# Optimization experiments

Measured on AMD Instinct MI355X. Metric: run time of the kernel, lower is better.

The kernel has to match this reference:

```python
import jax, jax.numpy as jnp
import numpy as np

UNITS = 512
SENSORY = 256
BATCH = 256
ODE_UNFOLDS = 6
EPSILON = 1e-8
ELAPSED_TIME = 1.0


def setup_inputs() -> dict:
    key = jax.random.key(0)
    ks = jax.random.split(key, 16)
    u = lambda k, shape, lo, hi: jax.random.uniform(k, shape, jnp.float32, lo, hi)
    pm1 = lambda k, shape: (jax.random.randint(k, shape, 0, 2).astype(jnp.float32) * 2.0 - 1.0)
    return {
        "x": jax.random.normal(ks[0], (BATCH, SENSORY), jnp.float32),
        "state": jax.random.normal(ks[1], (BATCH, UNITS), jnp.float32),
        "gleak": u(ks[2], (UNITS,), 0.001, 1.0),
        "vleak": u(ks[3], (UNITS,), -0.2, 0.2),
        "cm": u(ks[4], (UNITS,), 0.4, 0.6),
        "sigma": u(ks[5], (UNITS, UNITS), 3.0, 8.0),
        "mu": u(ks[6], (UNITS, UNITS), 0.3, 0.8),
        "w": u(ks[7], (UNITS, UNITS), 0.001, 1.0),
        "erev": pm1(ks[8], (UNITS, UNITS)),
        "sensory_sigma": u(ks[9], (SENSORY, UNITS), 3.0, 8.0),
        "sensory_mu": u(ks[10], (SENSORY, UNITS), 0.3, 0.8),
        "sensory_w": u(ks[11], (SENSORY, UNITS), 0.001, 1.0),
        "sensory_erev": pm1(ks[12], (SENSORY, UNITS)),
        "input_w": jnp.ones((SENSORY,), jnp.float32),
        "input_b": jnp.zeros((SENSORY,), jnp.float32),
        "output_w": jnp.ones((UNITS,), jnp.float32),
        "output_b": jnp.zeros((UNITS,), jnp.float32),
    }


def _gate(v_pre, mu, sigma):
    # v_pre: (B, P) broadcast against (P, Q) params -> (B, P, Q)
    return jax.nn.sigmoid(sigma * (v_pre[:, :, None] - mu))


def reference(x, state, gleak, vleak, cm, sigma, mu, w, erev,
              sensory_sigma, sensory_mu, sensory_w, sensory_erev,
              input_w, input_b, output_w, output_b):
    inputs = x * input_w + input_b  # (B, D)
    sens_act = sensory_w * _gate(inputs, sensory_mu, sensory_sigma)  # (B, D, N)
    w_num_sensory = jnp.sum(sens_act * sensory_erev, axis=1)  # (B, N)
    w_den_sensory = jnp.sum(sens_act, axis=1)                 # (B, N)

    cm_t = cm / ((ELAPSED_TIME + 0.001) / ODE_UNFOLDS)  # (N,)
    v_pre = state
    for _ in range(ODE_UNFOLDS):
        w_act = w * _gate(v_pre, mu, sigma)               # (B, N, N)
        w_num = jnp.sum(w_act * erev, axis=1) + w_num_sensory
        w_den = jnp.sum(w_act, axis=1) + w_den_sensory
        numerator = cm_t * v_pre + gleak * vleak + w_num
        denominator = cm_t + gleak + w_den
        v_pre = numerator / (denominator + EPSILON)

    outputs = v_pre * output_w + output_b
    return outputs, v_pre
```

## Files before the change

### kernel.cpp

```cpp
#include <hip/hip_runtime.h>

#define UNITS 512
#define SENSD 256
#define BATCH 256
#define BN (BATCH * UNITS)
#define LOG2E 1.44269504088896340736f
#define CMF (6.0f / 1.001f)

__device__ __forceinline__ float frcp(float x)  { return __builtin_amdgcn_rcpf(x); }
__device__ __forceinline__ float fexp2(float x) { return __builtin_amdgcn_exp2f(x); }

__global__ __launch_bounds__(256) void prep_kernel(
    const float* __restrict__ sigma, const float* __restrict__ mu,
    const float* __restrict__ w, const float* __restrict__ erev,
    const float* __restrict__ ssig, const float* __restrict__ smu,
    const float* __restrict__ sw, const float* __restrict__ serev,
    const float* __restrict__ gleak, const float* __restrict__ vleak,
    const float* __restrict__ cm,
    float4* __restrict__ fusedR, float4* __restrict__ fusedS,
    float4* __restrict__ cmg) {
  int idx = blockIdx.x * 256 + threadIdx.x;
  if (idx < UNITS * UNITS) {
    float s = sigma[idx], m = mu[idx], ww = w[idx], e = erev[idx];
    fusedR[idx] = make_float4(-s * LOG2E, s * m * LOG2E, ww, ww * e);
  } else {
    int j = idx - UNITS * UNITS;
    if (j < SENSD * UNITS) {
      float s = ssig[j], m = smu[j], ww = sw[j], e = serev[j];
      fusedS[j] = make_float4(-s * LOG2E, s * m * LOG2E, ww, ww * e);
    }
  }
  if (idx < UNITS) {
    float cmt = cm[idx] * CMF, gl = gleak[idx];
    cmg[idx] = make_float4(cmt, gl * vleak[idx], cmt + gl + 1e-8f, 0.f);
  }
}

__global__ __launch_bounds__(256) void sensory_kernel(
    const float* __restrict__ x, const float* __restrict__ in_w, const float* __restrict__ in_b,
    const float4* __restrict__ fusedS,
    float* __restrict__ snf, float* __restrict__ sdf) {
  __shared__ float xl[8][128];
  int bi = blockIdx.x;
  int phs = bi & 1, qt = (bi >> 1) & 7, bt = bi >> 4;
  int tid = threadIdx.x;
  for (int i = tid; i < 1024; i += 256) {
    int br = i >> 7, dl = i & 127;
    int d = phs * 128 + dl;
    xl[br][dl] = fmaf(x[(bt * 8 + br) * SENSD + d], in_w[d], in_b[d]);
  }
  __syncthreads();
  int ql = tid & 63, bg = tid >> 6;
  int q = qt * 64 + ql;
  int r0 = bg * 2;
  const float4* F = fusedS + (size_t)(phs * 128) * UNITS + q;
  float n0 = 0.f, dn0 = 0.f, n1 = 0.f, dn1 = 0.f;
  #pragma unroll 8
  for (int dd = 0; dd < 128; ++dd) {
    float4 f = F[(size_t)dd * UNITS];
    float v0 = xl[r0][dd], v1 = xl[r0 + 1][dd];
    float u0 = 1.0f + fexp2(fmaf(f.x, v0, f.y));
    float u1 = 1.0f + fexp2(fmaf(f.x, v1, f.y));
    float r = frcp(u0 * u1);
    float m = f.w * r, k = f.z * r;
    n0 = fmaf(m, u1, n0);  dn0 = fmaf(k, u1, dn0);
    n1 = fmaf(m, u0, n1);  dn1 = fmaf(k, u0, dn1);
  }
  int bp0 = (bt * 8 + r0) * UNITS + q;
  size_t o = (size_t)phs * BN + bp0;
  snf[o] = n0;         sdf[o] = dn0;
  snf[o + UNITS] = n1; sdf[o + UNITS] = dn1;
}

__global__ __launch_bounds__(256, 4) void unfold_kernel(
    const float4* __restrict__ fusedR, const float* __restrict__ vprev,
    const float* __restrict__ pn_in, const float* __restrict__ pd_in,
    const float* __restrict__ snf, const float* __restrict__ sdf,
    const float4* __restrict__ cmg,
    float* __restrict__ vout,
    float* __restrict__ pn_out, float* __restrict__ pd_out,
    int first) {
  __shared__ float vl[64][20];
  int bi = blockIdx.x;
  int ph = bi & 7, qt = (bi >> 3) & 7, bt = bi >> 6;
  int tid = threadIdx.x;
  if (first) {
    for (int i = tid; i < 1024; i += 256) {
      int br = i >> 6, pl = i & 63;
      vl[pl][br] = vprev[(bt * 16 + br) * UNITS + ph * 64 + pl];
    }
  } else {
    for (int i = tid; i < 1024; i += 256) {
      int br = i >> 6, pl = i & 63;
      int p = ph * 64 + pl;
      int bp = (bt * 16 + br) * UNITS + p;
      float num = ((pn_in[bp] + pn_in[BN + bp]) + (pn_in[2 * BN + bp] + pn_in[3 * BN + bp]))
                + ((pn_in[4 * BN + bp] + pn_in[5 * BN + bp]) + (pn_in[6 * BN + bp] + pn_in[7 * BN + bp]))
                + (snf[bp] + snf[BN + bp]);
      float den = ((pd_in[bp] + pd_in[BN + bp]) + (pd_in[2 * BN + bp] + pd_in[3 * BN + bp]))
                + ((pd_in[4 * BN + bp] + pd_in[5 * BN + bp]) + (pd_in[6 * BN + bp] + pd_in[7 * BN + bp]))
                + (sdf[bp] + sdf[BN + bp]);
      float4 c = cmg[p];
      float v = fmaf(c.x, vprev[bp], c.y + num) * frcp(c.z + den);
      vl[pl][br] = v;
      if (qt == 0) vout[bp] = v;
    }
  }
  __syncthreads();
  int ql = tid & 63, bg = tid >> 6;
  int q = qt * 64 + ql;
  int r0 = bg * 4;
  const float4* F = fusedR + (size_t)(ph * 64) * UNITS + q;
  float n0 = 0.f, n1 = 0.f, n2 = 0.f, n3 = 0.f;
  float d0 = 0.f, d1 = 0.f, d2 = 0.f, d3 = 0.f;
  #pragma unroll 8
  for (int pp = 0; pp < 64; ++pp) {
    float4 f = F[(size_t)pp * UNITS];
    float4 vv = *(const float4*)&vl[pp][r0];
    float u0 = 1.0f + fexp2(fmaf(f.x, vv.x, f.y));
    float u1 = 1.0f + fexp2(fmaf(f.x, vv.y, f.y));
    float u2 = 1.0f + fexp2(fmaf(f.x, vv.z, f.y));
    float u3 = 1.0f + fexp2(fmaf(f.x, vv.w, f.y));
    float rA = frcp(u0 * u1);
    float rB = frcp(u2 * u3);
    float mA = f.w * rA, kA = f.z * rA;
    float mB = f.w * rB, kB = f.z * rB;
    n0 = fmaf(mA, u1, n0);  d0 = fmaf(kA, u1, d0);
    n1 = fmaf(mA, u0, n1);  d1 = fmaf(kA, u0, d1);
    n2 = fmaf(mB, u3, n2);  d2 = fmaf(kB, u3, d2);
    n3 = fmaf(mB, u2, n3);  d3 = fmaf(kB, u2, d3);
  }
  int bp = (bt * 16 + r0) * UNITS + q;
  size_t o = (size_t)ph * BN + bp;
  pn_out[o] = n0;             pd_out[o] = d0;
  pn_out[o + UNITS] = n1;     pd_out[o + UNITS] = d1;
  pn_out[o + 2 * UNITS] = n2; pd_out[o + 2 * UNITS] = d2;
  pn_out[o + 3 * UNITS] = n3; pd_out[o + 3 * UNITS] = d3;
}

__global__ __launch_bounds__(256) void final_kernel(
    const float* __restrict__ vprev,
    const float* __restrict__ pn, const float* __restrict__ pd,
    const float* __restrict__ snf, const float* __restrict__ sdf,
    const float4* __restrict__ cmg,
    const float* __restrict__ ow, const float* __restrict__ ob,
    float* __restrict__ out) {
  int idx = blockIdx.x * 256 + threadIdx.x;
  if (idx >= BN) return;
  int p = idx & (UNITS - 1);
  float num = ((pn[idx] + pn[BN + idx]) + (pn[2 * BN + idx] + pn[3 * BN + idx]))
            + ((pn[4 * BN + idx] + pn[5 * BN + idx]) + (pn[6 * BN + idx] + pn[7 * BN + idx]))
            + (snf[idx] + snf[BN + idx]);
  float den = ((pd[idx] + pd[BN + idx]) + (pd[2 * BN + idx] + pd[3 * BN + idx]))
            + ((pd[4 * BN + idx] + pd[5 * BN + idx]) + (pd[6 * BN + idx] + pd[7 * BN + idx]))
            + (sdf[idx] + sdf[BN + idx]);
  float4 c = cmg[p];
  float v = fmaf(c.x, vprev[idx], c.y + num) * frcp(c.z + den);
  out[idx] = fmaf(v, ow[p], ob[p]);
  out[BN + idx] = v;
}

extern "C" void kernel_launch(void* const* d_in, const int* in_sizes, int n_in,
                              void* d_out, int out_size, void* d_ws, size_t ws_size,
                              hipStream_t stream) {
  (void)in_sizes; (void)n_in; (void)out_size; (void)ws_size;
  const float* x     = (const float*)d_in[0];
  const float* state = (const float*)d_in[1];
  const float* gleak = (const float*)d_in[2];
  const float* vleak = (const float*)d_in[3];
  const float* cm    = (const float*)d_in[4];
  const float* sigma = (const float*)d_in[5];
  const float* mu    = (const float*)d_in[6];
  const float* w     = (const float*)d_in[7];
  const float* erev  = (const float*)d_in[8];
  const float* ssig  = (const float*)d_in[9];
  const float* smu   = (const float*)d_in[10];
  const float* sw    = (const float*)d_in[11];
  const float* serev = (const float*)d_in[12];
  const float* in_w  = (const float*)d_in[13];
  const float* in_b  = (const float*)d_in[14];
  const float* out_w = (const float*)d_in[15];
  const float* out_b = (const float*)d_in[16];

  float* ws = (float*)d_ws;
  float4* fusedR = (float4*)(ws);
  float4* fusedS = (float4*)(ws + 1048576);
  float4* cmg    = (float4*)(ws + 1572864);
  float*  pnA    = ws + 1574912;
  float*  pdA    = ws + 2623488;
  float*  pnB    = ws + 3672064;
  float*  pdB    = ws + 4720640;
  float*  snf    = ws + 5769216;
  float*  sdf    = ws + 6031360;
  float*  vA     = ws + 6293504;
  float*  vB     = ws + 6424576;

  prep_kernel<<<1536, 256, 0, stream>>>(sigma, mu, w, erev, ssig, smu, sw, serev,
                                        gleak, vleak, cm, fusedR, fusedS, cmg);
  sensory_kernel<<<512, 256, 0, stream>>>(x, in_w, in_b, fusedS, snf, sdf);

  unfold_kernel<<<1024, 256, 0, stream>>>(fusedR, state, pnA, pdA, snf, sdf, cmg,
                                          vA, pnA, pdA, 1);
  unfold_kernel<<<1024, 256, 0, stream>>>(fusedR, state, pnA, pdA, snf, sdf, cmg,
                                          vA, pnB, pdB, 0);
  unfold_kernel<<<1024, 256, 0, stream>>>(fusedR, vA, pnB, pdB, snf, sdf, cmg,
                                          vB, pnA, pdA, 0);
  unfold_kernel<<<1024, 256, 0, stream>>>(fusedR, vB, pnA, pdA, snf, sdf, cmg,
                                          vA, pnB, pdB, 0);
  unfold_kernel<<<1024, 256, 0, stream>>>(fusedR, vA, pnB, pdB, snf, sdf, cmg,
                                          vB, pnA, pdA, 0);
  unfold_kernel<<<1024, 256, 0, stream>>>(fusedR, vB, pnA, pdA, snf, sdf, cmg,
                                          vA, pnB, pdB, 0);
  final_kernel<<<512, 256, 0, stream>>>(vA, pnB, pdB, snf, sdf, cmg,
                                        out_w, out_b, (float*)d_out);
}
```

Before: 161.2 us.

## Use packed FP32 FMAs with duplicated parameter layout in gate accumulation loops

Each gate parameter is now written twice (pairs duplicated into two float4 arrays), so the inner loops can use two-wide packed FMA (v_pk_fma_f32) over pairs of batch rows. The paired-reciprocal trick (one rcp for two gates plus extra multiplies) is replaced by one reciprocal per gate, relying on packed math to cut the VALU instruction count. In exchange, the parameter tensors double in size, so global/L2 traffic per iteration doubles, the unroll drops to 4, and twice as many transcendental rcp ops are issued.

```diff
diff --git a/kernel.cpp b/kernel.cpp
--- a/kernel.cpp
+++ b/kernel.cpp
@@ -7,8 +7,11 @@
 #define LOG2E 1.44269504088896340736f
 #define CMF (6.0f / 1.001f)
 
+typedef __attribute__((ext_vector_type(2))) float v2f;
+
 __device__ __forceinline__ float frcp(float x)  { return __builtin_amdgcn_rcpf(x); }
 __device__ __forceinline__ float fexp2(float x) { return __builtin_amdgcn_exp2f(x); }
+__device__ __forceinline__ v2f vfma(v2f a, v2f b, v2f c) { return __builtin_elementwise_fma(a, b, c); }
 
 __global__ __launch_bounds__(256) void prep_kernel(
     const float* __restrict__ sigma, const float* __restrict__ mu,
@@ -17,17 +20,22 @@
     const float* __restrict__ sw, const float* __restrict__ serev,
     const float* __restrict__ gleak, const float* __restrict__ vleak,
     const float* __restrict__ cm,
-    float4* __restrict__ fusedR, float4* __restrict__ fusedS,
+    float4* __restrict__ RA, float4* __restrict__ RB,
+    float4* __restrict__ SA, float4* __restrict__ SB,
     float4* __restrict__ cmg) {
   int idx = blockIdx.x * 256 + threadIdx.x;
   if (idx < UNITS * UNITS) {
     float s = sigma[idx], m = mu[idx], ww = w[idx], e = erev[idx];
-    fusedR[idx] = make_float4(-s * LOG2E, s * m * LOG2E, ww, ww * e);
+    float fx = -s * LOG2E, fy = s * m * LOG2E, we = ww * e;
+    RA[idx] = make_float4(fx, fx, fy, fy);
+    RB[idx] = make_float4(ww, ww, we, we);
   } else {
     int j = idx - UNITS * UNITS;
     if (j < SENSD * UNITS) {
       float s = ssig[j], m = smu[j], ww = sw[j], e = serev[j];
-      fusedS[j] = make_float4(-s * LOG2E, s * m * LOG2E, ww, ww * e);
+      float fx = -s * LOG2E, fy = s * m * LOG2E, we = ww * e;
+      SA[j] = make_float4(fx, fx, fy, fy);
+      SB[j] = make_float4(ww, ww, we, we);
     }
   }
   if (idx < UNITS) {
@@ -38,7 +46,7 @@
 
 __global__ __launch_bounds__(256) void sensory_kernel(
     const float* __restrict__ x, const float* __restrict__ in_w, const float* __restrict__ in_b,
-    const float4* __restrict__ fusedS,
+    const float4* __restrict__ SA, const float4* __restrict__ SB,
     float* __restrict__ snf, float* __restrict__ sdf) {
   __shared__ float xl[8][128];
   int bi = blockIdx.x;
@@ -53,27 +61,33 @@
   int ql = tid & 63, bg = tid >> 6;
   int q = qt * 64 + ql;
   int r0 = bg * 2;
-  const float4* F = fusedS + (size_t)(phs * 128) * UNITS + q;
-  float n0 = 0.f, dn0 = 0.f, n1 = 0.f, dn1 = 0.f;
-  #pragma unroll 8
+  const float4* FA = SA + (size_t)(phs * 128) * UNITS + q;
+  const float4* FB = SB + (size_t)(phs * 128) * UNITS + q;
+  const v2f one2 = {1.0f, 1.0f};
+  v2f n01 = {0.f, 0.f}, d01 = {0.f, 0.f};
+  #pragma unroll 4
   for (int dd = 0; dd < 128; ++dd) {
-    float4 f = F[(size_t)dd * UNITS];
-    float v0 = xl[r0][dd], v1 = xl[r0 + 1][dd];
-    float u0 = 1.0f + fexp2(fmaf(f.x, v0, f.y));
-    float u1 = 1.0f + fexp2(fmaf(f.x, v1, f.y));
-    float r = frcp(u0 * u1);
-    float m = f.w * r, k = f.z * r;
-    n0 = fmaf(m, u1, n0);  dn0 = fmaf(k, u1, dn0);
-    n1 = fmaf(m, u0, n1);  dn1 = fmaf(k, u0, dn1);
+    float4 fa = FA[(size_t)dd * UNITS];
+    float4 fb = FB[(size_t)dd * UNITS];
+    v2f fxx = {fa.x, fa.y}, fyy = {fa.z, fa.w};
+    v2f fzz = {fb.x, fb.y}, fww = {fb.z, fb.w};
+    v2f v01 = {xl[r0][dd], xl[r0 + 1][dd]};
+    v2f z01 = vfma(fxx, v01, fyy);
+    v2f t01; t01.x = fexp2(z01.x); t01.y = fexp2(z01.y);
+    v2f u01 = t01 + one2;
+    v2f s01; s01.x = frcp(u01.x); s01.y = frcp(u01.y);
+    n01 = vfma(fww, s01, n01);
+    d01 = vfma(fzz, s01, d01);
   }
   int bp0 = (bt * 8 + r0) * UNITS + q;
   size_t o = (size_t)phs * BN + bp0;
-  snf[o] = n0;         sdf[o] = dn0;
-  snf[o + UNITS] = n1; sdf[o + UNITS] = dn1;
+  snf[o] = n01.x;         sdf[o] = d01.x;
+  snf[o + UNITS] = n01.y; sdf[o + UNITS] = d01.y;
 }
 
 __global__ __launch_bounds__(256, 4) void unfold_kernel(
-    const float4* __restrict__ fusedR, const float* __restrict__ vprev,
+    const float4* __restrict__ RA, const float4* __restrict__ RB,
+    const float* __restrict__ vprev,
     const float* __restrict__ pn_in, const float* __restrict__ pd_in,
     const float* __restrict__ snf, const float* __restrict__ sdf,
     const float4* __restrict__ cmg,
@@ -110,32 +124,36 @@
   int ql = tid & 63, bg = tid >> 6;
   int q = qt * 64 + ql;
   int r0 = bg * 4;
-  const float4* F = fusedR + (size_t)(ph * 64) * UNITS + q;
-  float n0 = 0.f, n1 = 0.f, n2 = 0.f, n3 = 0.f;
-  float d0 = 0.f, d1 = 0.f, d2 = 0.f, d3 = 0.f;
-  #pragma unroll 8
+  const float4* FA = RA + (size_t)(ph * 64) * UNITS + q;
+  const float4* FB = RB + (size_t)(ph * 64) * UNITS + q;
+  const v2f one2 = {1.0f, 1.0f};
+  v2f n01 = {0.f, 0.f}, d01 = {0.f, 0.f};
+  v2f n23 = {0.f, 0.f}, d23 = {0.f, 0.f};
+  #pragma unroll 4
   for (int pp = 0; pp < 64; ++pp) {
-    float4 f = F[(size_t)pp * UNITS];
+    float4 fa = FA[(size_t)pp * UNITS];
+    float4 fb = FB[(size_t)pp * UNITS];
     float4 vv = *(const float4*)&vl[pp][r0];
-    float u0 = 1.0f + fexp2(fmaf(f.x, vv.x, f.y));
-    float u1 = 1.0f + fexp2(fmaf(f.x, vv.y, f.y));
-    float u2 = 1.0f + fexp2(fmaf(f.x, vv.z, f.y));
-    float u3 = 1.0f + fexp2(fmaf(f.x, vv.w, f.y));
-    float rA = frcp(u0 * u1);
-    float rB = frcp(u2 * u3);
-    float mA = f.w * rA, kA = f.z * rA;
-    float mB = f.w * rB, kB = f.z * rB;
-    n0 = fmaf(mA, u1, n0);  d0 = fmaf(kA, u1, d0);
-    n1 = fmaf(mA, u0, n1);  d1 = fmaf(kA, u0, d1);
-    n2 = fmaf(mB, u3, n2);  d2 = fmaf(kB, u3, d2);
-    n3 = fmaf(mB, u2, n3);  d3 = fmaf(kB, u2, d3);
+    v2f fxx = {fa.x, fa.y}, fyy = {fa.z, fa.w};
+    v2f fzz = {fb.x, fb.y}, fww = {fb.z, fb.w};
+    v2f v01 = {vv.x, vv.y}, v23 = {vv.z, vv.w};
+    v2f z01 = vfma(fxx, v01, fyy);
+    v2f z23 = vfma(fxx, v23, fyy);
+    v2f t01; t01.x = fexp2(z01.x); t01.y = fexp2(z01.y);
+    v2f t23; t23.x = fexp2(z23.x); t23.y = fexp2(z23.y);
+    v2f u01 = t01 + one2;
+    v2f u23 = t23 + one2;
+    v2f s01; s01.x = frcp(u01.x); s01.y = frcp(u01.y);
+    v2f s23; s23.x = frcp(u23.x); s23.y = frcp(u23.y);
+    n01 = vfma(fww, s01, n01);  d01 = vfma(fzz, s01, d01);
+    n23 = vfma(fww, s23, n23);  d23 = vfma(fzz, s23, d23);
   }
   int bp = (bt * 16 + r0) * UNITS + q;
   size_t o = (size_t)ph * BN + bp;
-  pn_out[o] = n0;             pd_out[o] = d0;
-  pn_out[o + UNITS] = n1;     pd_out[o + UNITS] = d1;
-  pn_out[o + 2 * UNITS] = n2; pd_out[o + 2 * UNITS] = d2;
-  pn_out[o + 3 * UNITS] = n3; pd_out[o + 3 * UNITS] = d3;
+  pn_out[o] = n01.x;             pd_out[o] = d01.x;
+  pn_out[o + UNITS] = n01.y;     pd_out[o + UNITS] = d01.y;
+  pn_out[o + 2 * UNITS] = n23.x; pd_out[o + 2 * UNITS] = d23.x;
+  pn_out[o + 3 * UNITS] = n23.y; pd_out[o + 3 * UNITS] = d23.y;
 }
 
 __global__ __launch_bounds__(256) void final_kernel(
@@ -183,33 +201,35 @@
   const float* out_b = (const float*)d_in[16];
 
   float* ws = (float*)d_ws;
-  float4* fusedR = (float4*)(ws);
-  float4* fusedS = (float4*)(ws + 1048576);
-  float4* cmg    = (float4*)(ws + 1572864);
-  float*  pnA    = ws + 1574912;
-  float*  pdA    = ws + 2623488;
-  float*  pnB    = ws + 3672064;
-  float*  pdB    = ws + 4720640;
-  float*  snf    = ws + 5769216;
-  float*  sdf    = ws + 6031360;
-  float*  vA     = ws + 6293504;
-  float*  vB     = ws + 6424576;
+  float4* RA  = (float4*)(ws);
+  float4* RB  = (float4*)(ws + 1048576);
+  float4* SA  = (float4*)(ws + 2097152);
+  float4* SB  = (float4*)(ws + 2621440);
+  float4* cmg = (float4*)(ws + 3145728);
+  float*  pnA = ws + 3147776;
+  float*  pdA = ws + 4196352;
+  float*  pnB = ws + 5244928;
+  float*  pdB = ws + 6293504;
+  float*  snf = ws + 7342080;
+  float*  sdf = ws + 7604224;
+  float*  vA  = ws + 7866368;
+  float*  vB  = ws + 7997440;
 
   prep_kernel<<<1536, 256, 0, stream>>>(sigma, mu, w, erev, ssig, smu, sw, serev,
-                                        gleak, vleak, cm, fusedR, fusedS, cmg);
-  sensory_kernel<<<512, 256, 0, stream>>>(x, in_w, in_b, fusedS, snf, sdf);
-
-  unfold_kernel<<<1024, 256, 0, stream>>>(fusedR, state, pnA, pdA, snf, sdf, cmg,
+                                        gleak, vleak, cm, RA, RB, SA, SB, cmg);
+  sensory_kernel<<<512, 256, 0, stream>>>(x, in_w, in_b, SA, SB, snf, sdf);
+
+  unfold_kernel<<<1024, 256, 0, stream>>>(RA, RB, state, pnA, pdA, snf, sdf, cmg,
                                           vA, pnA, pdA, 1);
-  unfold_kernel<<<1024, 256, 0, stream>>>(fusedR, state, pnA, pdA, snf, sdf, cmg,
+  unfold_kernel<<<1024, 256, 0, stream>>>(RA, RB, state, pnA, pdA, snf, sdf, cmg,
                                           vA, pnB, pdB, 0);
-  unfold_kernel<<<1024, 256, 0, stream>>>(fusedR, vA, pnB, pdB, snf, sdf, cmg,
+  unfold_kernel<<<1024, 256, 0, stream>>>(RA, RB, vA, pnB, pdB, snf, sdf, cmg,
                                           vB, pnA, pdA, 0);
-  unfold_kernel<<<1024, 256, 0, stream>>>(fusedR, vB, pnA, pdA, snf, sdf, cmg,
+  unfold_kernel<<<1024, 256, 0, stream>>>(RA, RB, vB, pnA, pdA, snf, sdf, cmg,
                                           vA, pnB, pdB, 0);
-  unfold_kernel<<<1024, 256, 0, stream>>>(fusedR, vA, pnB, pdB, snf, sdf, cmg,
+  unfold_kernel<<<1024, 256, 0, stream>>>(RA, RB, vA, pnB, pdB, snf, sdf, cmg,
                                           vB, pnA, pdA, 0);
-  unfold_kernel<<<1024, 256, 0, stream>>>(fusedR, vB, pnA, pdA, snf, sdf, cmg,
+  unfold_kernel<<<1024, 256, 0, stream>>>(RA, RB, vB, pnA, pdA, snf, sdf, cmg,
                                           vA, pnB, pdB, 0);
   final_kernel<<<512, 256, 0, stream>>>(vA, pnB, pdB, snf, sdf, cmg,
                                         out_w, out_b, (float*)d_out);
```

After: 171.0 us. 6.1% more time.
